# Kernel optimization log

Hardware: AMD Instinct MI355X
Metric: run time of the kernel (lower is better)

The kernel has to match this reference:

```python
import jax, jax.numpy as jnp
import numpy as np

NUM_FEATURES = 16
NUM_CLASSES = 4
HIDDEN = 128
NUM_LAYERS = 2
BN_EPS = 1e-5


def setup_inputs() -> dict:
    key = jax.random.key(0)
    ks = jax.random.split(key, 12)
    B, S, N, F, E = 8, 12, 5000, NUM_FEATURES, 40000
    H, L, C = HIDDEN, NUM_LAYERS, NUM_CLASSES
    x_seq = jax.random.normal(ks[0], (B, S, N, F), dtype=jnp.float32)
    edge_index = jax.random.randint(ks[1], (2, E), 0, N, dtype=jnp.int32)
    edge_weight = jax.random.uniform(ks[2], (E,), dtype=jnp.float32)
    def glorot(k, shape):
        fan_in, fan_out = shape[0], shape[-1]
        lim = jnp.sqrt(6.0 / (fan_in + fan_out)).astype(jnp.float32)
        return jax.random.uniform(k, shape, jnp.float32, -lim, lim)
    lin_in_W = glorot(ks[3], (F, H))
    lin_in_b = jnp.zeros((H,), jnp.float32)
    # per layer: 3 GCNConvs with weight [(H+H), H]
    convW = glorot(ks[4], (L, 3, 2 * H, H))
    convB = jnp.zeros((L, 3, H), jnp.float32)
    bn_gamma = jnp.ones((H,), jnp.float32)
    bn_beta = jnp.zeros((H,), jnp.float32)
    lin_out_W = glorot(ks[5], (H, C))
    lin_out_b = jnp.zeros((C,), jnp.float32)
    return {
        "x_seq": x_seq, "edge_index": edge_index, "edge_weight": edge_weight,
        "lin_in_W": lin_in_W, "lin_in_b": lin_in_b,
        "convW": convW, "convB": convB,
        "bn_gamma": bn_gamma, "bn_beta": bn_beta,
        "lin_out_W": lin_out_W, "lin_out_b": lin_out_b,
    }


def _batch_static_graph(edge_index, edge_weight, batch_size, num_nodes):
    E = edge_index.shape[1]
    shift = (jnp.arange(batch_size, dtype=edge_index.dtype) * num_nodes)  # [B]
    shift = jnp.repeat(shift, E)  # [B*E]
    bei = jnp.tile(edge_index, (1, batch_size)) + shift[None, :]
    bew = jnp.tile(edge_weight, batch_size)
    return bei, bew


def _gcn_norm(edge_index, edge_weight, num_nodes):
    # PyG GCNConv default: add self-loops (weight 1), sym normalization.
    loop = jnp.arange(num_nodes, dtype=edge_index.dtype)
    row = jnp.concatenate([edge_index[0], loop])
    col = jnp.concatenate([edge_index[1], loop])
    w = jnp.concatenate([edge_weight, jnp.ones((num_nodes,), edge_weight.dtype)])
    deg = jax.ops.segment_sum(w, col, num_segments=num_nodes)
    dis = jnp.where(deg > 0, jax.lax.rsqrt(jnp.where(deg > 0, deg, 1.0)), 0.0)
    norm = dis[row] * w * dis[col]
    return row, col, norm


def reference(x_seq, edge_index, edge_weight, lin_in_W, lin_in_b,
              convW, convB, bn_gamma, bn_beta, lin_out_W, lin_out_b):
    B, S, N, F = x_seq.shape
    H = lin_in_W.shape[1]
    L = convW.shape[0]
    bei, bew = _batch_static_graph(edge_index, edge_weight, B, N)
    total = B * N
    row, col, norm = _gcn_norm(bei, bew, total)
    # [S, total, F]
    xs = jnp.transpose(x_seq, (1, 0, 2, 3)).reshape(S, total, F)

    def gconv(x, W, b):
        xw = x @ W                                # [total, H]
        msg = norm[:, None] * xw[row]             # [E', H]
        return jax.ops.segment_sum(msg, col, num_segments=total) + b

    def step(h_all, x_t):
        x_t = jax.nn.relu(x_t @ lin_in_W + lin_in_b)
        new_h = []
        for l in range(L):
            h = h_all[l]
            combined = jnp.concatenate([x_t, h], axis=1)
            r = jax.nn.sigmoid(gconv(combined, convW[l, 0], convB[l, 0]))
            u = jax.nn.sigmoid(gconv(combined, convW[l, 1], convB[l, 1]))
            combined_r = jnp.concatenate([x_t, r * h], axis=1)
            c = jnp.tanh(gconv(combined_r, convW[l, 2], convB[l, 2]))
            h_new = u * h + (1.0 - u) * c
            new_h.append(h_new)
            x_t = h_new  # dropout is identity in eval mode
        return jnp.stack(new_h), None

    h0 = jnp.zeros((L, total, H), x_seq.dtype)
    h_all, _ = jax.lax.scan(step, h0, xs)
    h_final = h_all[-1]
    # BatchNorm over node dimension (training-mode batch statistics)
    mean = jnp.mean(h_final, axis=0)
    var = jnp.var(h_final, axis=0)
    h_final = (h_final - mean) * jax.lax.rsqrt(var + BN_EPS) * bn_gamma + bn_beta
    h_final = jax.nn.relu(h_final)
    out = h_final @ lin_out_W + lin_out_b            # [total, C]
    out = out.reshape(B, N, -1)
    return jax.nn.log_softmax(out, axis=-1)
```

## Files before the change

### kernel.cpp

```cpp
#include <hip/hip_runtime.h>
#include <cstdint>
#include <cstddef>

#define NN 5000
#define EE 40000
#define BATCH 8
#define SS 12
#define FF 16
#define HH 128
#define TOTAL 40000
#define CC 4


typedef __attribute__((ext_vector_type(8))) short short8;
typedef __attribute__((ext_vector_type(4))) float f32x4;

__device__ __forceinline__ unsigned short f2bf(float f) {
  union { float f; unsigned u; } v; v.f = f;
  unsigned r = v.u + 0x7fff + ((v.u >> 16) & 1);
  return (unsigned short)(r >> 16);
}
__device__ __forceinline__ float bf2f(unsigned short b) {
  union { unsigned u; float f; } v; v.u = ((unsigned)b) << 16;
  return v.f;
}
__device__ __forceinline__ float bflo(unsigned v) {
  union { unsigned u; float f; } x; x.u = v << 16; return x.f;
}
__device__ __forceinline__ float bfhi(unsigned v) {
  union { unsigned u; float f; } x; x.u = v & 0xffff0000u; return x.f;
}
__device__ __forceinline__ void qfma16(float* acc, uint4 qv, float ws) {
  unsigned wd[4] = {qv.x, qv.y, qv.z, qv.w};
#pragma unroll
  for (int d = 0; d < 4; d++) {
#pragma unroll
    for (int k = 0; k < 4; k++) {
      int q = (int)((signed char)(wd[d] >> (8 * k)));
      acc[d * 4 + k] += ws * (float)q;
    }
  }
}

__device__ __forceinline__ void gather_accum(const signed char* __restrict__ Gq,
                                             const float* __restrict__ sc,
                                             int e0, int e1,
                                             const int* __restrict__ csr_src,
                                             const float* __restrict__ csr_w,
                                             const float* __restrict__ dis,
                                             int n, int bb, int fo, float* acc) {
  float sn = dis[n]; sn *= sn;
  size_t rowSelf = (size_t)(n << 3) + bb;
#pragma unroll
  for (int k = 0; k < 16; k++) acc[k] = 0.f;
  {
    float ws = sn * sc[n];
    uint4 qv = *(const uint4*)&Gq[rowSelf * 128 + fo];
    qfma16(acc, qv, ws);
  }
  int e = e0;
  for (; e + 3 < e1; e += 4) {
    int s0 = csr_src[e], s1 = csr_src[e + 1];
    int s2 = csr_src[e + 2], s3 = csr_src[e + 3];
    float w0 = csr_w[e] * sc[s0];
    float w1 = csr_w[e + 1] * sc[s1];
    float w2 = csr_w[e + 2] * sc[s2];
    float w3 = csr_w[e + 3] * sc[s3];
    uint4 qa = *(const uint4*)&Gq[(((size_t)s0 << 3) + bb) * 128 + fo];
    uint4 qb = *(const uint4*)&Gq[(((size_t)s1 << 3) + bb) * 128 + fo];
    uint4 qc = *(const uint4*)&Gq[(((size_t)s2 << 3) + bb) * 128 + fo];
    uint4 qd = *(const uint4*)&Gq[(((size_t)s3 << 3) + bb) * 128 + fo];
    qfma16(acc, qa, w0);
    qfma16(acc, qb, w1);
    qfma16(acc, qc, w2);
    qfma16(acc, qd, w3);
  }
  for (; e < e1; e++) {
    int s0 = csr_src[e];
    float w0 = csr_w[e] * sc[s0];
    uint4 qa = *(const uint4*)&Gq[(((size_t)s0 << 3) + bb) * 128 + fo];
    qfma16(acc, qa, w0);
  }
}

__device__ __forceinline__ void gru_combine_store(const float* acc, const float* bp,
                                                  const unsigned short* __restrict__ u_in,
                                                  unsigned short* __restrict__ h_io,
                                                  size_t rowSelf, int fo,
                                                  uint4& o0, uint4& o1) {
  uint4 oo[2];
#pragma unroll
  for (int jj = 0; jj < 2; jj++) {
    uint4 uq = *(const uint4*)&u_in[rowSelf * 128 + fo + 8 * jj];
    uint4 hq = *(const uint4*)&h_io[rowSelf * 128 + fo + 8 * jj];
    float uv[8], hv[8];
    uv[0] = bflo(uq.x); uv[1] = bfhi(uq.x); uv[2] = bflo(uq.y); uv[3] = bfhi(uq.y);
    uv[4] = bflo(uq.z); uv[5] = bfhi(uq.z); uv[6] = bflo(uq.w); uv[7] = bfhi(uq.w);
    hv[0] = bflo(hq.x); hv[1] = bfhi(hq.x); hv[2] = bflo(hq.y); hv[3] = bfhi(hq.y);
    hv[4] = bflo(hq.z); hv[5] = bfhi(hq.z); hv[6] = bflo(hq.w); hv[7] = bfhi(hq.w);
    unsigned ow[4];
#pragma unroll
    for (int d = 0; d < 4; d++) {
      float v0 = acc[8 * jj + 2 * d]     + bp[8 * jj + 2 * d];
      float v1 = acc[8 * jj + 2 * d + 1] + bp[8 * jj + 2 * d + 1];
      float c0 = 1.0f - 2.0f / (__expf(2.0f * v0) + 1.0f);
      float c1 = 1.0f - 2.0f / (__expf(2.0f * v1) + 1.0f);
      float n0 = uv[2 * d] * hv[2 * d] + (1.0f - uv[2 * d]) * c0;
      float n1 = uv[2 * d + 1] * hv[2 * d + 1] + (1.0f - uv[2 * d + 1]) * c1;
      ow[d] = (unsigned)f2bf(n0) | ((unsigned)f2bf(n1) << 16);
    }
    oo[jj].x = ow[0]; oo[jj].y = ow[1]; oo[jj].z = ow[2]; oo[jj].w = ow[3];
    *(uint4*)&h_io[rowSelf * 128 + fo + 8 * jj] = oo[jj];
  }
  o0 = oo[0]; o1 = oo[1];
}


__global__ void deg_cnt_kernel(const int* __restrict__ ei, const float* __restrict__ ew,
                               float* __restrict__ deg, int* __restrict__ cnt) {
  int e = blockIdx.x * 256 + threadIdx.x;
  if (e < EE) {
    int col = ei[EE + e];
    atomicAdd(&deg[col], ew[e]);
    atomicAdd(&cnt[col], 1);
  }
}

__global__ void dis_kernel(const float* __restrict__ deg, float* __restrict__ dis) {
  int n = blockIdx.x * 256 + threadIdx.x;
  if (n < NN) dis[n] = rsqrtf(deg[n] + 1.0f);
}

__global__ void scan_kernel(const int* __restrict__ cnt, int* __restrict__ offs) {
  __shared__ int part[256];
  const int CH = (NN + 255) / 256;
  int tid = threadIdx.x;
  int base = tid * CH;
  int s = 0;
  for (int i = 0; i < CH; i++) { int idx = base + i; if (idx < NN) s += cnt[idx]; }
  part[tid] = s;
  __syncthreads();
  for (int off = 1; off < 256; off <<= 1) {
    int v = (tid >= off) ? part[tid - off] : 0;
    __syncthreads();
    part[tid] += v;
    __syncthreads();
  }
  int run = (tid == 0) ? 0 : part[tid - 1];
  for (int i = 0; i < CH; i++) {
    int idx = base + i;
    if (idx < NN) { offs[idx] = run; run += cnt[idx]; }
  }
  if (tid == 255) offs[NN] = run;
}

__global__ void fill_csr_kernel(const int* __restrict__ ei, const float* __restrict__ ew,
                                const float* __restrict__ dis, const int* __restrict__ offs,
                                int* __restrict__ cursor, int* __restrict__ csr_src,
                                float* __restrict__ csr_w) {
  int e = blockIdx.x * 256 + threadIdx.x;
  if (e < EE) {
    int row = ei[e], col = ei[EE + e];
    int pos = offs[col] + atomicAdd(&cursor[col], 1);
    csr_src[pos] = row;
    csr_w[pos] = dis[row] * ew[e] * dis[col];
  }
}


__global__ void prepack_kernel(const float* __restrict__ convW, unsigned short* __restrict__ Wp) {
  int idx = blockIdx.x * 256 + threadIdx.x;
  int lane = idx & 63;
  int ks = (idx >> 6) & 7;
  int nt = (idx >> 9) & 7;
  int g = idx >> 12;
  const float* W = convW + (size_t)g * 256 * 128;
  int n = nt * 16 + (lane & 15);
  int k0 = ks * 32 + (lane >> 4) * 8;
  unsigned short v[8];
#pragma unroll
  for (int j = 0; j < 8; j++) v[j] = f2bf(W[(size_t)(k0 + j) * 128 + n]);
  *(uint4*)(Wp + (size_t)idx * 8) = *(const uint4*)v;
}


__global__ __launch_bounds__(256) void lin_in_kernel(const float* __restrict__ x_seq,
                                                     const float* __restrict__ W,
                                                     const float* __restrict__ b,
                                                     unsigned short* __restrict__ xt, int t) {
  int idx = blockIdx.x * 256 + threadIdx.x;
  int row = idx >> 4, fh = idx & 15;
  int n = row >> 3, bb = row & 7;
  const float* xp = x_seq + (((size_t)bb * SS + t) * NN + n) * FF;
  float4 a0 = *(const float4*)&b[fh * 8];
  float4 a1 = *(const float4*)&b[fh * 8 + 4];
#pragma unroll
  for (int ff = 0; ff < FF; ff++) {
    float xv = xp[ff];
    float4 w0 = *(const float4*)&W[ff * HH + fh * 8];
    float4 w1 = *(const float4*)&W[ff * HH + fh * 8 + 4];
    a0.x += xv * w0.x; a0.y += xv * w0.y; a0.z += xv * w0.z; a0.w += xv * w0.w;
    a1.x += xv * w1.x; a1.y += xv * w1.y; a1.z += xv * w1.z; a1.w += xv * w1.w;
  }
  uint4 o;
  o.x = (unsigned)f2bf(fmaxf(a0.x, 0.f)) | ((unsigned)f2bf(fmaxf(a0.y, 0.f)) << 16);
  o.y = (unsigned)f2bf(fmaxf(a0.z, 0.f)) | ((unsigned)f2bf(fmaxf(a0.w, 0.f)) << 16);
  o.z = (unsigned)f2bf(fmaxf(a1.x, 0.f)) | ((unsigned)f2bf(fmaxf(a1.y, 0.f)) << 16);
  o.w = (unsigned)f2bf(fmaxf(a1.z, 0.f)) | ((unsigned)f2bf(fmaxf(a1.w, 0.f)) << 16);
  *(uint4*)&xt[(size_t)row * 128 + fh * 8] = o;
}


template <int MT, int NTW, int HALVES, int NTHREADS>
__device__ __forceinline__ void gemm_body(const unsigned short* As, unsigned short* Cs,
                                          float* sInv,
                                          const unsigned short* __restrict__ Wp,
                                          signed char* __restrict__ qA,
                                          signed char* __restrict__ qB,
                                          float* __restrict__ sA,
                                          float* __restrict__ sB,
                                          int rowBase, int tid) {
  constexpr int NWAVES = NTHREADS / 64;
  constexpr int NC = NTW * 16 * NWAVES;
  constexpr int R = MT * 16;
  int wv = tid >> 6, lane = tid & 63;
  int m = lane & 15, q = lane >> 4;
  f32x4 acc[MT][NTW];
#pragma unroll
  for (int i = 0; i < MT; i++)
#pragma unroll
    for (int j = 0; j < NTW; j++) acc[i][j] = (f32x4)(0.0f);
  const unsigned short* wbase = Wp + ((size_t)(wv * NTW) * 8 * 64 + lane) * 8;
#pragma unroll
  for (int ks = 0; ks < 8; ks++) {
    short8 a[MT];
#pragma unroll
    for (int mt = 0; mt < MT; mt++)
      a[mt] = *(const short8*)&As[(mt * 16 + m) * 264 + ks * 32 + q * 8];
#pragma unroll
    for (int nt = 0; nt < NTW; nt++) {
      short8 b = *(const short8*)(wbase + (size_t)(nt * 8 + ks) * 64 * 8);
#pragma unroll
      for (int mt = 0; mt < MT; mt++)
        acc[mt][nt] = __builtin_amdgcn_mfma_f32_16x16x32_bf16(a[mt], b, acc[mt][nt], 0, 0, 0);
    }
  }
  constexpr int CST = NC + 8;
#pragma unroll
  for (int mt = 0; mt < MT; mt++)
#pragma unroll
    for (int nt = 0; nt < NTW; nt++) {
      int col = (wv * NTW + nt) * 16 + m;
#pragma unroll
      for (int i = 0; i < 4; i++)
        Cs[(mt * 16 + q * 4 + i) * CST + col] = f2bf(acc[mt][nt][i]);
    }
  __syncthreads();
  constexpr int G = (R / 8) * HALVES;
  static_assert(G <= NWAVES, "one wave per quant group");
  if (wv < G) {
    int node = wv / HALVES, half = wv % HALVES;
    int c0 = half * 128 + lane * 2;
    float mx = 0.f;
#pragma unroll
    for (int r = 0; r < 8; r++) {
      const unsigned short* rp = &Cs[(node * 8 + r) * CST + c0];
      mx = fmaxf(mx, fmaxf(fabsf(bf2f(rp[0])), fabsf(bf2f(rp[1]))));
    }
#pragma unroll
    for (int off = 32; off; off >>= 1) mx = fmaxf(mx, __shfl_down(mx, off));
    if (lane == 0) {
      sInv[wv] = (mx > 0.f) ? (127.0f / mx) : 0.f;
      int gn = (rowBase >> 3) + node;
      float scv = mx * (1.0f / 127.0f);
      if (HALVES == 2) { if (half == 0) sA[gn] = scv; else sB[gn] = scv; }
      else sA[gn] = scv;
    }
  }
  __syncthreads();
  constexpr int CPQ = NC / 16;
  for (int c = tid; c < R * CPQ; c += NTHREADS) {
    int row = c / CPQ, cc = c % CPQ;
    int node = row >> 3;
    int half = (HALVES == 2) ? (cc >> 3) : 0;
    float inv = sInv[node * HALVES + half];
    const unsigned short* p = &Cs[row * CST + cc * 16];
    unsigned ow[4];
#pragma unroll
    for (int d = 0; d < 4; d++) {
      unsigned w = 0;
#pragma unroll
      for (int k = 0; k < 4; k++) {
        int qv = __float2int_rn(bf2f(p[d * 4 + k]) * inv);
        w |= ((unsigned)(qv & 255)) << (8 * k);
      }
      ow[d] = w;
    }
    signed char* dst = (half ? qB : qA) + (size_t)(rowBase + row) * 128 + (cc & 7) * 16;
    uint4 v; v.x = ow[0]; v.y = ow[1]; v.z = ow[2]; v.w = ow[3];
    *(uint4*)dst = v;
  }
}


template <int NTW, int HALVES>
__global__ __launch_bounds__(512) void gemm_mfma_q(const unsigned short* __restrict__ A1,
                                                   const unsigned short* __restrict__ A2,
                                                   const unsigned short* __restrict__ Wp,
                                                   signed char* __restrict__ qA,
                                                   signed char* __restrict__ qB,
                                                   float* __restrict__ sA,
                                                   float* __restrict__ sB) {
  __shared__ unsigned short As[32 * 264];
  __shared__ unsigned short Cs[32 * 264];
  __shared__ float sInv[8];
  int rowBase = blockIdx.x * 32;
  int tid = threadIdx.x;
  for (int c = tid; c < 1024; c += 512) {
    int row = c >> 5; int rest = c & 31; int half = rest >> 4; int sub = rest & 15;
    const unsigned short* src = (half ? A2 : A1) + ((size_t)(rowBase + row) * 128 + sub * 8);
    *(uint4*)&As[row * 264 + half * 128 + sub * 8] = *(const uint4*)src;
  }
  __syncthreads();
  gemm_body<2, NTW, HALVES, 512>(As, Cs, sInv, Wp, qA, qB, sA, sB, rowBase, tid);
}


__global__ __launch_bounds__(512, 8) void fused_cand_q(
    const signed char* __restrict__ GqR, const signed char* __restrict__ GqU,
    const float* __restrict__ sR, const float* __restrict__ sU,
    const int* __restrict__ offs, const int* __restrict__ csr_src,
    const float* __restrict__ csr_w, const float* __restrict__ dis,
    const float* __restrict__ bRU, const unsigned short* __restrict__ h,
    unsigned short* __restrict__ u_out,
    const unsigned short* __restrict__ A1, const unsigned short* __restrict__ Wp,
    signed char* __restrict__ Cq, float* __restrict__ sC) {
  __shared__ unsigned short As[32 * 264];
  __shared__ unsigned short Cs[32 * 136];
  __shared__ float sInv[8];
  int tid = threadIdx.x;
  int wv = tid >> 6, lane = tid & 63;
  int rowBase = blockIdx.x * 32, gn0 = rowBase >> 3;
  int bb = lane >> 3, fo = (lane & 7) << 4;
  int node8 = wv >> 1, half = wv & 1;
  int n = gn0 + node8;
  int e0 = offs[n], e1 = offs[n + 1];
  {
    int row = tid >> 4, sub = tid & 15;
    *(uint4*)&As[row * 264 + sub * 8] =
        *(const uint4*)&A1[(size_t)(rowBase + row) * 128 + sub * 8];
  }
  float acc[16];
  gather_accum(half ? GqU : GqR, half ? sU : sR, e0, e1, csr_src, csr_w, dis, n, bb, fo, acc);
  const float* bias = bRU + half * 128 + fo;
  size_t rowSelf = ((size_t)n << 3) + bb;
  if (half == 0) {
    int lr = node8 * 8 + bb;
#pragma unroll
    for (int jj = 0; jj < 2; jj++) {
      uint4 hq = *(const uint4*)&h[rowSelf * 128 + fo + 8 * jj];
      float hv[8];
      hv[0] = bflo(hq.x); hv[1] = bfhi(hq.x); hv[2] = bflo(hq.y); hv[3] = bfhi(hq.y);
      hv[4] = bflo(hq.z); hv[5] = bfhi(hq.z); hv[6] = bflo(hq.w); hv[7] = bfhi(hq.w);
      unsigned ow[4];
#pragma unroll
      for (int d = 0; d < 4; d++) {
        float s0 = 1.0f / (1.0f + __expf(-(acc[8 * jj + 2 * d]     + bias[8 * jj + 2 * d])));
        float s1 = 1.0f / (1.0f + __expf(-(acc[8 * jj + 2 * d + 1] + bias[8 * jj + 2 * d + 1])));
        ow[d] = (unsigned)f2bf(s0 * hv[2 * d]) | ((unsigned)f2bf(s1 * hv[2 * d + 1]) << 16);
      }
      uint4 o; o.x = ow[0]; o.y = ow[1]; o.z = ow[2]; o.w = ow[3];
      *(uint4*)&As[lr * 264 + 128 + fo + 8 * jj] = o;
    }
  } else {
#pragma unroll
    for (int jj = 0; jj < 2; jj++) {
      unsigned ow[4];
#pragma unroll
      for (int d = 0; d < 4; d++) {
        float s0 = 1.0f / (1.0f + __expf(-(acc[8 * jj + 2 * d]     + bias[8 * jj + 2 * d])));
        float s1 = 1.0f / (1.0f + __expf(-(acc[8 * jj + 2 * d + 1] + bias[8 * jj + 2 * d + 1])));
        ow[d] = (unsigned)f2bf(s0) | ((unsigned)f2bf(s1) << 16);
      }
      uint4 o; o.x = ow[0]; o.y = ow[1]; o.z = ow[2]; o.w = ow[3];
      *(uint4*)&u_out[rowSelf * 128 + fo + 8 * jj] = o;
    }
  }
  __syncthreads();
  gemm_body<2, 1, 1, 512>(As, Cs, sInv, Wp, Cq, Cq, sC, sC, rowBase, tid);
}


__global__ __launch_bounds__(512, 8) void fused_gates_q(
    const signed char* __restrict__ Cq, const float* __restrict__ sC,
    const int* __restrict__ offs, const int* __restrict__ csr_src,
    const float* __restrict__ csr_w, const float* __restrict__ dis,
    const float* __restrict__ bC, const unsigned short* __restrict__ u_in,
    unsigned short* __restrict__ h_io,
    const unsigned short* __restrict__ A2src, const unsigned short* __restrict__ Wp,
    signed char* __restrict__ GqRo, signed char* __restrict__ GqUo,
    float* __restrict__ sRo, float* __restrict__ sUo) {
  __shared__ unsigned short As[32 * 264];
  __shared__ unsigned short Cs[32 * 264];
  __shared__ float sInv[8];
  int tid = threadIdx.x;
  int wv = tid >> 6, lane = tid & 63;
  int rowBase = blockIdx.x * 32, gn0 = rowBase >> 3;
  int bb = lane >> 3, fo = (lane & 7) << 4;
  if (wv >= 4) {
    int t2 = tid - 256;
    for (int c = t2; c < 512; c += 256) {
      int row = c >> 4, sub = c & 15;
      *(uint4*)&As[row * 264 + 128 + sub * 8] =
          *(const uint4*)&A2src[(size_t)(rowBase + row) * 128 + sub * 8];
    }
  } else {
    int node8 = wv;
    int n = gn0 + node8;
    int e0 = offs[n], e1 = offs[n + 1];
    float acc[16];
    gather_accum(Cq, sC, e0, e1, csr_src, csr_w, dis, n, bb, fo, acc);
    size_t rowSelf = ((size_t)n << 3) + bb;
    uint4 o0, o1;
    gru_combine_store(acc, bC + fo, u_in, h_io, rowSelf, fo, o0, o1);
    int lr = node8 * 8 + bb;
    *(uint4*)&As[lr * 264 + fo] = o0;
    *(uint4*)&As[lr * 264 + fo + 8] = o1;
  }
  __syncthreads();
  gemm_body<2, 2, 2, 512>(As, Cs, sInv, Wp, GqRo, GqUo, sRo, sUo, rowBase, tid);
}


__global__ __launch_bounds__(512, 8) void fused_gates_lin_q(
    const signed char* __restrict__ Cq, const float* __restrict__ sC,
    const int* __restrict__ offs, const int* __restrict__ csr_src,
    const float* __restrict__ csr_w, const float* __restrict__ dis,
    const float* __restrict__ bC, const unsigned short* __restrict__ u_in,
    unsigned short* __restrict__ h_io,
    const float* __restrict__ x_seq, const float* __restrict__ Win,
    const float* __restrict__ bin, unsigned short* __restrict__ xt_out,
    const unsigned short* __restrict__ A2src, const unsigned short* __restrict__ Wp,
    signed char* __restrict__ GqRo, signed char* __restrict__ GqUo,
    float* __restrict__ sRo, float* __restrict__ sUo, int t_next) {
  __shared__ unsigned short As[32 * 264];
  __shared__ unsigned short Cs[32 * 264];
  __shared__ float sInv[8];
  int tid = threadIdx.x;
  int wv = tid >> 6, lane = tid & 63;
  int rowBase = blockIdx.x * 32, gn0 = rowBase >> 3;
  int bb = lane >> 3, fo = (lane & 7) << 4;
  if (wv < 4) {
    int node8 = wv;
    int n = gn0 + node8;
    int e0 = offs[n], e1 = offs[n + 1];
    float acc[16];
    gather_accum(Cq, sC, e0, e1, csr_src, csr_w, dis, n, bb, fo, acc);
    size_t rowSelf = ((size_t)n << 3) + bb;
    uint4 o0, o1;
    gru_combine_store(acc, bC + fo, u_in, h_io, rowSelf, fo, o0, o1);
  } else {
    int t2 = tid - 256;
    for (int c = t2; c < 512; c += 256) {
      int row = c >> 4, sub = c & 15;
      *(uint4*)&As[row * 264 + 128 + sub * 8] =
          *(const uint4*)&A2src[(size_t)(rowBase + row) * 128 + sub * 8];
    }
    for (int c = t2; c < 512; c += 256) {
      int row = c >> 4, fh = c & 15;
      int grow = rowBase + row;
      int n2 = grow >> 3, bbv = grow & 7;
      const float* xp = x_seq + (((size_t)bbv * SS + t_next) * NN + n2) * FF;
      float4 a0 = *(const float4*)&bin[fh * 8];
      float4 a1 = *(const float4*)&bin[fh * 8 + 4];
#pragma unroll
      for (int ff = 0; ff < FF; ff++) {
        float xv = xp[ff];
        float4 w0 = *(const float4*)&Win[ff * HH + fh * 8];
        float4 w1 = *(const float4*)&Win[ff * HH + fh * 8 + 4];
        a0.x += xv * w0.x; a0.y += xv * w0.y; a0.z += xv * w0.z; a0.w += xv * w0.w;
        a1.x += xv * w1.x; a1.y += xv * w1.y; a1.z += xv * w1.z; a1.w += xv * w1.w;
      }
      uint4 o;
      o.x = (unsigned)f2bf(fmaxf(a0.x, 0.f)) | ((unsigned)f2bf(fmaxf(a0.y, 0.f)) << 16);
      o.y = (unsigned)f2bf(fmaxf(a0.z, 0.f)) | ((unsigned)f2bf(fmaxf(a0.w, 0.f)) << 16);
      o.z = (unsigned)f2bf(fmaxf(a1.x, 0.f)) | ((unsigned)f2bf(fmaxf(a1.y, 0.f)) << 16);
      o.w = (unsigned)f2bf(fmaxf(a1.z, 0.f)) | ((unsigned)f2bf(fmaxf(a1.w, 0.f)) << 16);
      *(uint4*)&As[row * 264 + fh * 8] = o;
      *(uint4*)&xt_out[(size_t)grow * 128 + fh * 8] = o;
    }
  }
  __syncthreads();
  gemm_body<2, 2, 2, 512>(As, Cs, sInv, Wp, GqRo, GqUo, sRo, sUo, rowBase, tid);
}


__global__ __launch_bounds__(256) void scatter_c_update_q(
    const signed char* __restrict__ Cq, const float* __restrict__ sC,
    const int* __restrict__ offs, const int* __restrict__ csr_src,
    const float* __restrict__ csr_w, const float* __restrict__ dis,
    const float* __restrict__ bC, const unsigned short* __restrict__ u,
    unsigned short* __restrict__ h) {
  int tid = threadIdx.x;
  int wv = tid >> 6, lane = tid & 63;
  int n = blockIdx.x * 4 + wv;
  int bb = lane >> 3;
  int fo = (lane & 7) << 4;
  int e0 = offs[n], e1 = offs[n + 1];
  float acc[16];
  gather_accum(Cq, sC, e0, e1, csr_src, csr_w, dis, n, bb, fo, acc);
  size_t rowSelf = (size_t)(n << 3) + bb;
  uint4 o0, o1;
  gru_combine_store(acc, bC + fo, u, h, rowSelf, fo, o0, o1);
}


__global__ __launch_bounds__(256) void bn_stats_kernel(const unsigned short* __restrict__ h,
                                                       float* __restrict__ sums) {
  __shared__ float ls[512];
  int tid = threadIdx.x;
  float s = 0.f, sq = 0.f;
  for (size_t idx = (size_t)blockIdx.x * 256 + tid; idx < (size_t)TOTAL * HH;
       idx += (size_t)gridDim.x * 256) {
    float v = bf2f(h[idx]);
    s += v; sq += v * v;
  }
  ls[tid] = s; ls[256 + tid] = sq;
  __syncthreads();
  if (tid < 128) {
    atomicAdd(&sums[tid], ls[tid] + ls[tid + 128]);
    atomicAdd(&sums[128 + tid], ls[256 + tid] + ls[256 + tid + 128]);
  }
}


__global__ __launch_bounds__(256) void final_kernel(const unsigned short* __restrict__ h,
                                                    const float* __restrict__ sums,
                                                    const float* __restrict__ gamma,
                                                    const float* __restrict__ beta,
                                                    const float* __restrict__ Wout,
                                                    const float* __restrict__ bout,
                                                    float* __restrict__ out) {
  int wid = threadIdx.x >> 6, lane = threadIdx.x & 63;
  int row = blockIdx.x * 4 + wid;
  if (row >= TOTAL) return;
  const float inv = 1.0f / (float)TOTAL;
  float p0 = 0.f, p1 = 0.f, p2 = 0.f, p3 = 0.f;
#pragma unroll
  for (int jj = 0; jj < 2; jj++) {
    int j = lane + jj * 64;
    float mean = sums[j] * inv;
    float var = sums[128 + j] * inv - mean * mean;
    float hn = (bf2f(h[(size_t)row * HH + j]) - mean) * rsqrtf(var + 1e-5f) * gamma[j] + beta[j];
    hn = fmaxf(hn, 0.0f);
    p0 += hn * Wout[j * 4 + 0];
    p1 += hn * Wout[j * 4 + 1];
    p2 += hn * Wout[j * 4 + 2];
    p3 += hn * Wout[j * 4 + 3];
  }
  for (int off = 32; off; off >>= 1) {
    p0 += __shfl_down(p0, off);
    p1 += __shfl_down(p1, off);
    p2 += __shfl_down(p2, off);
    p3 += __shfl_down(p3, off);
  }
  if (lane == 0) {
    p0 += bout[0]; p1 += bout[1]; p2 += bout[2]; p3 += bout[3];
    float m = fmaxf(fmaxf(p0, p1), fmaxf(p2, p3));
    float e = __expf(p0 - m) + __expf(p1 - m) + __expf(p2 - m) + __expf(p3 - m);
    float lse = m + __logf(e);
    int bb = row & 7, n = row >> 3;
    float* o = out + ((size_t)bb * NN + n) * 4;
    o[0] = p0 - lse; o[1] = p1 - lse; o[2] = p2 - lse; o[3] = p3 - lse;
  }
}


extern "C" void kernel_launch(void* const* d_in, const int* in_sizes, int n_in,
                              void* d_out, int out_size, void* d_ws, size_t ws_size,
                              hipStream_t stream) {
  const float* x_seq = (const float*)d_in[0];
  const int* ei      = (const int*)d_in[1];
  const float* ew    = (const float*)d_in[2];
  const float* Win   = (const float*)d_in[3];
  const float* bin   = (const float*)d_in[4];
  const float* convW = (const float*)d_in[5];
  const float* convB = (const float*)d_in[6];
  const float* gamma = (const float*)d_in[7];
  const float* beta  = (const float*)d_in[8];
  const float* Wout  = (const float*)d_in[9];
  const float* bout  = (const float*)d_in[10];
  float* out = (float*)d_out;

  char* ws = (char*)d_ws;
  size_t off = 0;
  auto alloc = [&](size_t bytes) {
    void* p = ws + off;
    off += (bytes + 1023) & ~(size_t)1023;
    return p;
  };
  float* deg     = (float*)alloc(NN * 4);
  float* dis     = (float*)alloc(NN * 4);
  int*   cnt     = (int*)alloc(NN * 4);
  int*   offs    = (int*)alloc((NN + 1) * 4);
  int*   cursor  = (int*)alloc(NN * 4);
  int*   csr_src = (int*)alloc(EE * 4);
  float* csr_w   = (float*)alloc(EE * 4);
  float* sums    = (float*)alloc(256 * 4);
  float* sR      = (float*)alloc(NN * 4);
  float* sU      = (float*)alloc(NN * 4);
  float* sC      = (float*)alloc(NN * 4);
  unsigned short* Wp = (unsigned short*)alloc(6 * 32768 * 2);
  const size_t NH = (size_t)TOTAL * HH;
  unsigned short* h0 = (unsigned short*)alloc(NH * 2);
  unsigned short* h1 = (unsigned short*)alloc(NH * 2);
  unsigned short* xt = (unsigned short*)alloc(NH * 2);
  unsigned short* ub = (unsigned short*)alloc(NH * 2);
  signed char* GqR = (signed char*)alloc(NH);
  signed char* GqU = (signed char*)alloc(NH);
  signed char* Cq  = (signed char*)alloc(NH);

  hipMemsetAsync(deg, 0, NN * 4, stream);
  hipMemsetAsync(cnt, 0, NN * 4, stream);
  hipMemsetAsync(cursor, 0, NN * 4, stream);
  hipMemsetAsync(sums, 0, 256 * 4, stream);
  hipMemsetAsync(h0, 0, NH * 2, stream);
  hipMemsetAsync(h1, 0, NH * 2, stream);

  deg_cnt_kernel<<<(EE + 255) / 256, 256, 0, stream>>>(ei, ew, deg, cnt);
  dis_kernel<<<(NN + 255) / 256, 256, 0, stream>>>(deg, dis);
  scan_kernel<<<1, 256, 0, stream>>>(cnt, offs);
  fill_csr_kernel<<<(EE + 255) / 256, 256, 0, stream>>>(ei, ew, dis, offs, cursor, csr_src, csr_w);
  prepack_kernel<<<24576 / 256, 256, 0, stream>>>(convW, Wp);

  const unsigned short* Wg0 = Wp;
  const unsigned short* Wc0 = Wp + (size_t)2 * 32768;
  const unsigned short* Wg1 = Wp + (size_t)3 * 32768;
  const unsigned short* Wc1 = Wp + (size_t)5 * 32768;
  const float* bRU0 = convB;
  const float* bC0  = convB + 2 * HH;
  const float* bRU1 = convB + 3 * HH;
  const float* bC1  = convB + 5 * HH;

  lin_in_kernel<<<TOTAL * 16 / 256, 256, 0, stream>>>(x_seq, Win, bin, xt, 0);
  gemm_mfma_q<2, 2><<<TOTAL / 32, 512, 0, stream>>>(xt, h0, Wg0, GqR, GqU, sR, sU);

  for (int t = 0; t < SS; t++) {
    fused_cand_q<<<TOTAL / 32, 512, 0, stream>>>(GqR, GqU, sR, sU, offs, csr_src, csr_w,
                                                 dis, bRU0, h0, ub, xt, Wc0, Cq, sC);
    fused_gates_q<<<TOTAL / 32, 512, 0, stream>>>(Cq, sC, offs, csr_src, csr_w, dis,
                                                  bC0, ub, h0, h1, Wg1, GqR, GqU, sR, sU);
    fused_cand_q<<<TOTAL / 32, 512, 0, stream>>>(GqR, GqU, sR, sU, offs, csr_src, csr_w,
                                                 dis, bRU1, h1, ub, h0, Wc1, Cq, sC);
    if (t < SS - 1) {
      fused_gates_lin_q<<<TOTAL / 32, 512, 0, stream>>>(Cq, sC, offs, csr_src, csr_w, dis,
                                                        bC1, ub, h1, x_seq, Win, bin, xt,
                                                        h0, Wg0, GqR, GqU, sR, sU, t + 1);
    } else {
      scatter_c_update_q<<<NN / 4, 256, 0, stream>>>(Cq, sC, offs, csr_src, csr_w,
                                                     dis, bC1, ub, h1);
    }
  }

  bn_stats_kernel<<<256, 256, 0, stream>>>(h1, sums);
  final_kernel<<<TOTAL / 4, 256, 0, stream>>>(h1, sums, gamma, beta, Wout, bout, out);
}
```

Before: 1.539 ms.

## Defer update-gate aggregation to gates kernel and quantize directly from MFMA registers

```diff
diff --git a/kernel.cpp b/kernel.cpp
--- a/kernel.cpp
+++ b/kernel.cpp
@@ -83,19 +83,16 @@
   }
 }
 
-__device__ __forceinline__ void gru_combine_store(const float* acc, const float* bp,
-                                                  const unsigned short* __restrict__ u_in,
-                                                  unsigned short* __restrict__ h_io,
-                                                  size_t rowSelf, int fo,
-                                                  uint4& o0, uint4& o1) {
+__device__ __forceinline__ void gru_combine_f32u(const float* acc, const float* bp,
+                                                 const float* uv,
+                                                 unsigned short* __restrict__ h_io,
+                                                 size_t rowSelf, int fo,
+                                                 uint4& o0, uint4& o1) {
   uint4 oo[2];
 #pragma unroll
   for (int jj = 0; jj < 2; jj++) {
-    uint4 uq = *(const uint4*)&u_in[rowSelf * 128 + fo + 8 * jj];
     uint4 hq = *(const uint4*)&h_io[rowSelf * 128 + fo + 8 * jj];
-    float uv[8], hv[8];
-    uv[0] = bflo(uq.x); uv[1] = bfhi(uq.x); uv[2] = bflo(uq.y); uv[3] = bfhi(uq.y);
-    uv[4] = bflo(uq.z); uv[5] = bfhi(uq.z); uv[6] = bflo(uq.w); uv[7] = bfhi(uq.w);
+    float hv[8];
     hv[0] = bflo(hq.x); hv[1] = bfhi(hq.x); hv[2] = bflo(hq.y); hv[3] = bfhi(hq.y);
     hv[4] = bflo(hq.z); hv[5] = bfhi(hq.z); hv[6] = bflo(hq.w); hv[7] = bfhi(hq.w);
     unsigned ow[4];
@@ -105,8 +102,9 @@
       float v1 = acc[8 * jj + 2 * d + 1] + bp[8 * jj + 2 * d + 1];
       float c0 = 1.0f - 2.0f / (__expf(2.0f * v0) + 1.0f);
       float c1 = 1.0f - 2.0f / (__expf(2.0f * v1) + 1.0f);
-      float n0 = uv[2 * d] * hv[2 * d] + (1.0f - uv[2 * d]) * c0;
-      float n1 = uv[2 * d + 1] * hv[2 * d + 1] + (1.0f - uv[2 * d + 1]) * c1;
+      float u0 = uv[8 * jj + 2 * d], u1 = uv[8 * jj + 2 * d + 1];
+      float n0 = u0 * hv[2 * d] + (1.0f - u0) * c0;
+      float n1 = u1 * hv[2 * d + 1] + (1.0f - u1) * c1;
       ow[d] = (unsigned)f2bf(n0) | ((unsigned)f2bf(n1) << 16);
     }
     oo[jj].x = ow[0]; oo[jj].y = ow[1]; oo[jj].z = ow[2]; oo[jj].w = ow[3];
@@ -212,8 +210,7 @@
 
 
 template <int MT, int NTW, int HALVES, int NTHREADS>
-__device__ __forceinline__ void gemm_body(const unsigned short* As, unsigned short* Cs,
-                                          float* sInv,
+__device__ __forceinline__ void gemm_body(const unsigned short* As, float* gmax,
                                           const unsigned short* __restrict__ Wp,
                                           signed char* __restrict__ qA,
                                           signed char* __restrict__ qB,
@@ -221,8 +218,8 @@
                                           float* __restrict__ sB,
                                           int rowBase, int tid) {
   constexpr int NWAVES = NTHREADS / 64;
-  constexpr int NC = NTW * 16 * NWAVES;
-  constexpr int R = MT * 16;
+  constexpr int WPG = NWAVES / HALVES;
+  static_assert(MT == 2, "node mapping assumes 32-row tile");
   int wv = tid >> 6, lane = tid & 63;
   int m = lane & 15, q = lane >> 4;
   f32x4 acc[MT][NTW];
@@ -245,60 +242,55 @@
         acc[mt][nt] = __builtin_amdgcn_mfma_f32_16x16x32_bf16(a[mt], b, acc[mt][nt], 0, 0, 0);
     }
   }
-  constexpr int CST = NC + 8;
-#pragma unroll
-  for (int mt = 0; mt < MT; mt++)
+  float mxa = 0.f, mxb = 0.f;
+#pragma unroll
+  for (int nt = 0; nt < NTW; nt++)
+#pragma unroll
+    for (int i = 0; i < 4; i++) {
+      mxa = fmaxf(mxa, fabsf(acc[0][nt][i]));
+      mxb = fmaxf(mxb, fabsf(acc[1][nt][i]));
+    }
+#pragma unroll
+  for (int off = 16; off; off >>= 1) {
+    mxa = fmaxf(mxa, __shfl_down(mxa, off));
+    mxb = fmaxf(mxb, __shfl_down(mxb, off));
+  }
+  if (lane == 0)  { gmax[wv * 4 + 0] = mxa; gmax[wv * 4 + 2] = mxb; }
+  if (lane == 32) { gmax[wv * 4 + 1] = mxa; gmax[wv * 4 + 3] = mxb; }
+  __syncthreads();
+  if (tid < 4 * HALVES) {
+    int node = (HALVES == 2) ? (tid >> 1) : tid;
+    int half = (HALVES == 2) ? (tid & 1) : 0;
+    float g = 0.f;
+#pragma unroll
+    for (int w = 0; w < WPG; w++) g = fmaxf(g, gmax[(half * WPG + w) * 4 + node]);
+    float* sp = half ? sB : sA;
+    sp[(rowBase >> 3) + node] = g * (1.0f / 127.0f);
+  }
+  int half = (HALVES == 2) ? (wv / WPG) : 0;
+  int qh = q >> 1;
+  float ga = 0.f, gb = 0.f;
+#pragma unroll
+  for (int w = 0; w < WPG; w++) {
+    ga = fmaxf(ga, gmax[(half * WPG + w) * 4 + qh]);
+    gb = fmaxf(gb, gmax[(half * WPG + w) * 4 + 2 + qh]);
+  }
+  float invA = (ga > 0.f) ? (127.0f / ga) : 0.f;
+  float invB = (gb > 0.f) ? (127.0f / gb) : 0.f;
+  signed char* qbase = (half ? qB : qA);
+#pragma unroll
+  for (int mt = 0; mt < MT; mt++) {
+    float inv = mt ? invB : invA;
 #pragma unroll
     for (int nt = 0; nt < NTW; nt++) {
-      int col = (wv * NTW + nt) * 16 + m;
-#pragma unroll
-      for (int i = 0; i < 4; i++)
-        Cs[(mt * 16 + q * 4 + i) * CST + col] = f2bf(acc[mt][nt][i]);
-    }
-  __syncthreads();
-  constexpr int G = (R / 8) * HALVES;
-  static_assert(G <= NWAVES, "one wave per quant group");
-  if (wv < G) {
-    int node = wv / HALVES, half = wv % HALVES;
-    int c0 = half * 128 + lane * 2;
-    float mx = 0.f;
-#pragma unroll
-    for (int r = 0; r < 8; r++) {
-      const unsigned short* rp = &Cs[(node * 8 + r) * CST + c0];
-      mx = fmaxf(mx, fmaxf(fabsf(bf2f(rp[0])), fabsf(bf2f(rp[1]))));
-    }
-#pragma unroll
-    for (int off = 32; off; off >>= 1) mx = fmaxf(mx, __shfl_down(mx, off));
-    if (lane == 0) {
-      sInv[wv] = (mx > 0.f) ? (127.0f / mx) : 0.f;
-      int gn = (rowBase >> 3) + node;
-      float scv = mx * (1.0f / 127.0f);
-      if (HALVES == 2) { if (half == 0) sA[gn] = scv; else sB[gn] = scv; }
-      else sA[gn] = scv;
-    }
-  }
-  __syncthreads();
-  constexpr int CPQ = NC / 16;
-  for (int c = tid; c < R * CPQ; c += NTHREADS) {
-    int row = c / CPQ, cc = c % CPQ;
-    int node = row >> 3;
-    int half = (HALVES == 2) ? (cc >> 3) : 0;
-    float inv = sInv[node * HALVES + half];
-    const unsigned short* p = &Cs[row * CST + cc * 16];
-    unsigned ow[4];
-#pragma unroll
-    for (int d = 0; d < 4; d++) {
-      unsigned w = 0;
-#pragma unroll
-      for (int k = 0; k < 4; k++) {
-        int qv = __float2int_rn(bf2f(p[d * 4 + k]) * inv);
-        w |= ((unsigned)(qv & 255)) << (8 * k);
+      int colq = (wv * NTW + nt) * 16 + m - half * 128;
+      signed char* dst = qbase + (size_t)(rowBase + mt * 16 + q * 4) * 128 + colq;
+#pragma unroll
+      for (int i = 0; i < 4; i++) {
+        int qv = __float2int_rn(acc[mt][nt][i] * inv);
+        dst[(size_t)i * 128] = (signed char)qv;
       }
-      ow[d] = w;
-    }
-    signed char* dst = (half ? qB : qA) + (size_t)(rowBase + row) * 128 + (cc & 7) * 16;
-    uint4 v; v.x = ow[0]; v.y = ow[1]; v.z = ow[2]; v.w = ow[3];
-    *(uint4*)dst = v;
+    }
   }
 }
 
@@ -312,8 +304,7 @@
                                                    float* __restrict__ sA,
                                                    float* __restrict__ sB) {
   __shared__ unsigned short As[32 * 264];
-  __shared__ unsigned short Cs[32 * 264];
-  __shared__ float sInv[8];
+  __shared__ float gmax[32];
   int rowBase = blockIdx.x * 32;
   int tid = threadIdx.x;
   for (int c = tid; c < 1024; c += 512) {
@@ -322,87 +313,19 @@
     *(uint4*)&As[row * 264 + half * 128 + sub * 8] = *(const uint4*)src;
   }
   __syncthreads();
-  gemm_body<2, NTW, HALVES, 512>(As, Cs, sInv, Wp, qA, qB, sA, sB, rowBase, tid);
+  gemm_body<2, NTW, HALVES, 512>(As, gmax, Wp, qA, qB, sA, sB, rowBase, tid);
 }
 
 
 __global__ __launch_bounds__(512, 8) void fused_cand_q(
-    const signed char* __restrict__ GqR, const signed char* __restrict__ GqU,
-    const float* __restrict__ sR, const float* __restrict__ sU,
+    const signed char* __restrict__ GqR, const float* __restrict__ sR,
     const int* __restrict__ offs, const int* __restrict__ csr_src,
     const float* __restrict__ csr_w, const float* __restrict__ dis,
-    const float* __restrict__ bRU, const unsigned short* __restrict__ h,
-    unsigned short* __restrict__ u_out,
+    const float* __restrict__ bR, const unsigned short* __restrict__ h,
     const unsigned short* __restrict__ A1, const unsigned short* __restrict__ Wp,
     signed char* __restrict__ Cq, float* __restrict__ sC) {
   __shared__ unsigned short As[32 * 264];
-  __shared__ unsigned short Cs[32 * 136];
-  __shared__ float sInv[8];
-  int tid = threadIdx.x;
-  int wv = tid >> 6, lane = tid & 63;
-  int rowBase = blockIdx.x * 32, gn0 = rowBase >> 3;
-  int bb = lane >> 3, fo = (lane & 7) << 4;
-  int node8 = wv >> 1, half = wv & 1;
-  int n = gn0 + node8;
-  int e0 = offs[n], e1 = offs[n + 1];
-  {
-    int row = tid >> 4, sub = tid & 15;
-    *(uint4*)&As[row * 264 + sub * 8] =
-        *(const uint4*)&A1[(size_t)(rowBase + row) * 128 + sub * 8];
-  }
-  float acc[16];
-  gather_accum(half ? GqU : GqR, half ? sU : sR, e0, e1, csr_src, csr_w, dis, n, bb, fo, acc);
-  const float* bias = bRU + half * 128 + fo;
-  size_t rowSelf = ((size_t)n << 3) + bb;
-  if (half == 0) {
-    int lr = node8 * 8 + bb;
-#pragma unroll
-    for (int jj = 0; jj < 2; jj++) {
-      uint4 hq = *(const uint4*)&h[rowSelf * 128 + fo + 8 * jj];
-      float hv[8];
-      hv[0] = bflo(hq.x); hv[1] = bfhi(hq.x); hv[2] = bflo(hq.y); hv[3] = bfhi(hq.y);
-      hv[4] = bflo(hq.z); hv[5] = bfhi(hq.z); hv[6] = bflo(hq.w); hv[7] = bfhi(hq.w);
-      unsigned ow[4];
-#pragma unroll
-      for (int d = 0; d < 4; d++) {
-        float s0 = 1.0f / (1.0f + __expf(-(acc[8 * jj + 2 * d]     + bias[8 * jj + 2 * d])));
-        float s1 = 1.0f / (1.0f + __expf(-(acc[8 * jj + 2 * d + 1] + bias[8 * jj + 2 * d + 1])));
-        ow[d] = (unsigned)f2bf(s0 * hv[2 * d]) | ((unsigned)f2bf(s1 * hv[2 * d + 1]) << 16);
-      }
-      uint4 o; o.x = ow[0]; o.y = ow[1]; o.z = ow[2]; o.w = ow[3];
-      *(uint4*)&As[lr * 264 + 128 + fo + 8 * jj] = o;
-    }
-  } else {
-#pragma unroll
-    for (int jj = 0; jj < 2; jj++) {
-      unsigned ow[4];
-#pragma unroll
-      for (int d = 0; d < 4; d++) {
-        float s0 = 1.0f / (1.0f + __expf(-(acc[8 * jj + 2 * d]     + bias[8 * jj + 2 * d])));
-        float s1 = 1.0f / (1.0f + __expf(-(acc[8 * jj + 2 * d + 1] + bias[8 * jj + 2 * d + 1])));
-        ow[d] = (unsigned)f2bf(s0) | ((unsigned)f2bf(s1) << 16);
-      }
-      uint4 o; o.x = ow[0]; o.y = ow[1]; o.z = ow[2]; o.w = ow[3];
-      *(uint4*)&u_out[rowSelf * 128 + fo + 8 * jj] = o;
-    }
-  }
-  __syncthreads();
-  gemm_body<2, 1, 1, 512>(As, Cs, sInv, Wp, Cq, Cq, sC, sC, rowBase, tid);
-}
-
-
-__global__ __launch_bounds__(512, 8) void fused_gates_q(
-    const signed char* __restrict__ Cq, const float* __restrict__ sC,
-    const int* __restrict__ offs, const int* __restrict__ csr_src,
-    const float* __restrict__ csr_w, const float* __restrict__ dis,
-    const float* __restrict__ bC, const unsigned short* __restrict__ u_in,
-    unsigned short* __restrict__ h_io,
-    const unsigned short* __restrict__ A2src, const unsigned short* __restrict__ Wp,
-    signed char* __restrict__ GqRo, signed char* __restrict__ GqUo,
-    float* __restrict__ sRo, float* __restrict__ sUo) {
-  __shared__ unsigned short As[32 * 264];
-  __shared__ unsigned short Cs[32 * 264];
-  __shared__ float sInv[8];
+  __shared__ float gmax[32];
   int tid = threadIdx.x;
   int wv = tid >> 6, lane = tid & 63;
   int rowBase = blockIdx.x * 32, gn0 = rowBase >> 3;
@@ -411,32 +334,98 @@
     int t2 = tid - 256;
     for (int c = t2; c < 512; c += 256) {
       int row = c >> 4, sub = c & 15;
-      *(uint4*)&As[row * 264 + 128 + sub * 8] =
-          *(const uint4*)&A2src[(size_t)(rowBase + row) * 128 + sub * 8];
+      *(uint4*)&As[row * 264 + sub * 8] =
+          *(const uint4*)&A1[(size_t)(rowBase + row) * 128 + sub * 8];
     }
   } else {
     int node8 = wv;
     int n = gn0 + node8;
     int e0 = offs[n], e1 = offs[n + 1];
     float acc[16];
+    gather_accum(GqR, sR, e0, e1, csr_src, csr_w, dis, n, bb, fo, acc);
+    size_t rowSelf = ((size_t)n << 3) + bb;
+    int lr = node8 * 8 + bb;
+#pragma unroll
+    for (int jj = 0; jj < 2; jj++) {
+      uint4 hq = *(const uint4*)&h[rowSelf * 128 + fo + 8 * jj];
+      float hv[8];
+      hv[0] = bflo(hq.x); hv[1] = bfhi(hq.x); hv[2] = bflo(hq.y); hv[3] = bfhi(hq.y);
+      hv[4] = bflo(hq.z); hv[5] = bfhi(hq.z); hv[6] = bflo(hq.w); hv[7] = bfhi(hq.w);
+      unsigned ow[4];
+#pragma unroll
+      for (int d = 0; d < 4; d++) {
+        float s0 = 1.0f / (1.0f + __expf(-(acc[8 * jj + 2 * d]     + bR[fo + 8 * jj + 2 * d])));
+        float s1 = 1.0f / (1.0f + __expf(-(acc[8 * jj + 2 * d + 1] + bR[fo + 8 * jj + 2 * d + 1])));
+        ow[d] = (unsigned)f2bf(s0 * hv[2 * d]) | ((unsigned)f2bf(s1 * hv[2 * d + 1]) << 16);
+      }
+      uint4 o; o.x = ow[0]; o.y = ow[1]; o.z = ow[2]; o.w = ow[3];
+      *(uint4*)&As[lr * 264 + 128 + fo + 8 * jj] = o;
+    }
+  }
+  __syncthreads();
+  gemm_body<2, 1, 1, 512>(As, gmax, Wp, Cq, Cq, sC, sC, rowBase, tid);
+}
+
+
+__global__ __launch_bounds__(512, 8) void fused_gates_q(
+    const signed char* __restrict__ Cq, const float* __restrict__ sC,
+    const signed char* __restrict__ GqU, const float* __restrict__ sU,
+    const int* __restrict__ offs, const int* __restrict__ csr_src,
+    const float* __restrict__ csr_w, const float* __restrict__ dis,
+    const float* __restrict__ bC, const float* __restrict__ bU,
+    unsigned short* __restrict__ h_io,
+    const unsigned short* __restrict__ A2src, const unsigned short* __restrict__ Wp,
+    signed char* __restrict__ GqRo, signed char* __restrict__ GqUo,
+    float* __restrict__ sRo, float* __restrict__ sUo) {
+  __shared__ unsigned short As[32 * 264];
+  __shared__ float uls[4][64][17];
+  __shared__ float gmax[32];
+  int tid = threadIdx.x;
+  int wv = tid >> 6, lane = tid & 63;
+  int rowBase = blockIdx.x * 32, gn0 = rowBase >> 3;
+  int bb = lane >> 3, fo = (lane & 7) << 4;
+  int node8 = wv & 3;
+  int n = gn0 + node8;
+  int e0 = offs[n], e1 = offs[n + 1];
+  float acc[16];
+  if (wv < 4) {
     gather_accum(Cq, sC, e0, e1, csr_src, csr_w, dis, n, bb, fo, acc);
+  } else {
+    gather_accum(GqU, sU, e0, e1, csr_src, csr_w, dis, n, bb, fo, acc);
+#pragma unroll
+    for (int k = 0; k < 16; k++)
+      uls[node8][lane][k] = 1.0f / (1.0f + __expf(-(acc[k] + bU[fo + k])));
+  }
+  __syncthreads();
+  if (wv < 4) {
+    float uv[16];
+#pragma unroll
+    for (int k = 0; k < 16; k++) uv[k] = uls[node8][lane][k];
     size_t rowSelf = ((size_t)n << 3) + bb;
     uint4 o0, o1;
-    gru_combine_store(acc, bC + fo, u_in, h_io, rowSelf, fo, o0, o1);
+    gru_combine_f32u(acc, bC + fo, uv, h_io, rowSelf, fo, o0, o1);
     int lr = node8 * 8 + bb;
     *(uint4*)&As[lr * 264 + fo] = o0;
     *(uint4*)&As[lr * 264 + fo + 8] = o1;
-  }
-  __syncthreads();
-  gemm_body<2, 2, 2, 512>(As, Cs, sInv, Wp, GqRo, GqUo, sRo, sUo, rowBase, tid);
+  } else {
+    int t2 = tid - 256;
+    for (int c = t2; c < 512; c += 256) {
+      int row = c >> 4, sub = c & 15;
+      *(uint4*)&As[row * 264 + 128 + sub * 8] =
+          *(const uint4*)&A2src[(size_t)(rowBase + row) * 128 + sub * 8];
+    }
+  }
+  __syncthreads();
+  gemm_body<2, 2, 2, 512>(As, gmax, Wp, GqRo, GqUo, sRo, sUo, rowBase, tid);
 }
 
 
 __global__ __launch_bounds__(512, 8) void fused_gates_lin_q(
     const signed char* __restrict__ Cq, const float* __restrict__ sC,
+    const signed char* __restrict__ GqU, const float* __restrict__ sU,
     const int* __restrict__ offs, const int* __restrict__ csr_src,
     const float* __restrict__ csr_w, const float* __restrict__ dis,
-    const float* __restrict__ bC, const unsigned short* __restrict__ u_in,
+    const float* __restrict__ bC, const float* __restrict__ bU,
     unsigned short* __restrict__ h_io,
     const float* __restrict__ x_seq, const float* __restrict__ Win,
     const float* __restrict__ bin, unsigned short* __restrict__ xt_out,
@@ -444,21 +433,32 @@
     signed char* __restrict__ GqRo, signed char* __restrict__ GqUo,
     float* __restrict__ sRo, float* __restrict__ sUo, int t_next) {
   __shared__ unsigned short As[32 * 264];
-  __shared__ unsigned short Cs[32 * 264];
-  __shared__ float sInv[8];
+  __shared__ float uls[4][64][17];
+  __shared__ float gmax[32];
   int tid = threadIdx.x;
   int wv = tid >> 6, lane = tid & 63;
   int rowBase = blockIdx.x * 32, gn0 = rowBase >> 3;
   int bb = lane >> 3, fo = (lane & 7) << 4;
+  int node8 = wv & 3;
+  int n = gn0 + node8;
+  int e0 = offs[n], e1 = offs[n + 1];
+  float acc[16];
   if (wv < 4) {
-    int node8 = wv;
-    int n = gn0 + node8;
-    int e0 = offs[n], e1 = offs[n + 1];
-    float acc[16];
     gather_accum(Cq, sC, e0, e1, csr_src, csr_w, dis, n, bb, fo, acc);
+  } else {
+    gather_accum(GqU, sU, e0, e1, csr_src, csr_w, dis, n, bb, fo, acc);
+#pragma unroll
+    for (int k = 0; k < 16; k++)
+      uls[node8][lane][k] = 1.0f / (1.0f + __expf(-(acc[k] + bU[fo + k])));
+  }
+  __syncthreads();
+  if (wv < 4) {
+    float uv[16];
+#pragma unroll
+    for (int k = 0; k < 16; k++) uv[k] = uls[node8][lane][k];
     size_t rowSelf = ((size_t)n << 3) + bb;
     uint4 o0, o1;
-    gru_combine_store(acc, bC + fo, u_in, h_io, rowSelf, fo, o0, o1);
+    gru_combine_f32u(acc, bC + fo, uv, h_io, rowSelf, fo, o0, o1);
   } else {
     int t2 = tid - 256;
     for (int c = t2; c < 512; c += 256) {
@@ -491,27 +491,43 @@
     }
   }
   __syncthreads();
-  gemm_body<2, 2, 2, 512>(As, Cs, sInv, Wp, GqRo, GqUo, sRo, sUo, rowBase, tid);
-}
-
-
-__global__ __launch_bounds__(256) void scatter_c_update_q(
+  gemm_body<2, 2, 2, 512>(As, gmax, Wp, GqRo, GqUo, sRo, sUo, rowBase, tid);
+}
+
+
+__global__ __launch_bounds__(256) void scatter_c_update2(
     const signed char* __restrict__ Cq, const float* __restrict__ sC,
+    const signed char* __restrict__ GqU, const float* __restrict__ sU,
     const int* __restrict__ offs, const int* __restrict__ csr_src,
     const float* __restrict__ csr_w, const float* __restrict__ dis,
-    const float* __restrict__ bC, const unsigned short* __restrict__ u,
+    const float* __restrict__ bC, const float* __restrict__ bU,
     unsigned short* __restrict__ h) {
+  __shared__ float uls[2][64][17];
   int tid = threadIdx.x;
   int wv = tid >> 6, lane = tid & 63;
-  int n = blockIdx.x * 4 + wv;
+  int which = wv & 1;
+  int n = blockIdx.x * 2 + which;
   int bb = lane >> 3;
   int fo = (lane & 7) << 4;
   int e0 = offs[n], e1 = offs[n + 1];
   float acc[16];
-  gather_accum(Cq, sC, e0, e1, csr_src, csr_w, dis, n, bb, fo, acc);
-  size_t rowSelf = (size_t)(n << 3) + bb;
-  uint4 o0, o1;
-  gru_combine_store(acc, bC + fo, u, h, rowSelf, fo, o0, o1);
+  if (wv < 2) {
+    gather_accum(Cq, sC, e0, e1, csr_src, csr_w, dis, n, bb, fo, acc);
+  } else {
+    gather_accum(GqU, sU, e0, e1, csr_src, csr_w, dis, n, bb, fo, acc);
+#pragma unroll
+    for (int k = 0; k < 16; k++)
+      uls[which][lane][k] = 1.0f / (1.0f + __expf(-(acc[k] + bU[fo + k])));
+  }
+  __syncthreads();
+  if (wv < 2) {
+    float uv[16];
+#pragma unroll
+    for (int k = 0; k < 16; k++) uv[k] = uls[which][lane][k];
+    size_t rowSelf = (size_t)(n << 3) + bb;
+    uint4 o0, o1;
+    gru_combine_f32u(acc, bC + fo, uv, h, rowSelf, fo, o0, o1);
+  }
 }
 
 
@@ -607,18 +623,21 @@
   int*   csr_src = (int*)alloc(EE * 4);
   float* csr_w   = (float*)alloc(EE * 4);
   float* sums    = (float*)alloc(256 * 4);
-  float* sR      = (float*)alloc(NN * 4);
-  float* sU      = (float*)alloc(NN * 4);
+  float* sR0     = (float*)alloc(NN * 4);
+  float* sU0     = (float*)alloc(NN * 4);
+  float* sR1     = (float*)alloc(NN * 4);
+  float* sU1     = (float*)alloc(NN * 4);
   float* sC      = (float*)alloc(NN * 4);
   unsigned short* Wp = (unsigned short*)alloc(6 * 32768 * 2);
   const size_t NH = (size_t)TOTAL * HH;
   unsigned short* h0 = (unsigned short*)alloc(NH * 2);
   unsigned short* h1 = (unsigned short*)alloc(NH * 2);
   unsigned short* xt = (unsigned short*)alloc(NH * 2);
-  unsigned short* ub = (unsigned short*)alloc(NH * 2);
-  signed char* GqR = (signed char*)alloc(NH);
-  signed char* GqU = (signed char*)alloc(NH);
-  signed char* Cq  = (signed char*)alloc(NH);
+  signed char* GqR0 = (signed char*)alloc(NH);
+  signed char* GqU0 = (signed char*)alloc(NH);
+  signed char* GqR1 = (signed char*)alloc(NH);
+  signed char* GqU1 = (signed char*)alloc(NH);
+  signed char* Cq   = (signed char*)alloc(NH);
 
   hipMemsetAsync(deg, 0, NN * 4, stream);
   hipMemsetAsync(cnt, 0, NN * 4, stream);
@@ -637,28 +656,32 @@
   const unsigned short* Wc0 = Wp + (size_t)2 * 32768;
   const unsigned short* Wg1 = Wp + (size_t)3 * 32768;
   const unsigned short* Wc1 = Wp + (size_t)5 * 32768;
-  const float* bRU0 = convB;
-  const float* bC0  = convB + 2 * HH;
-  const float* bRU1 = convB + 3 * HH;
-  const float* bC1  = convB + 5 * HH;
+  const float* bR0 = convB;
+  const float* bU0 = convB + 128;
+  const float* bC0 = convB + 2 * HH;
+  const float* bR1 = convB + 3 * HH;
+  const float* bU1 = convB + 3 * HH + 128;
+  const float* bC1 = convB + 5 * HH;
 
   lin_in_kernel<<<TOTAL * 16 / 256, 256, 0, stream>>>(x_seq, Win, bin, xt, 0);
-  gemm_mfma_q<2, 2><<<TOTAL / 32, 512, 0, stream>>>(xt, h0, Wg0, GqR, GqU, sR, sU);
+  gemm_mfma_q<2, 2><<<TOTAL / 32, 512, 0, stream>>>(xt, h0, Wg0, GqR0, GqU0, sR0, sU0);
 
   for (int t = 0; t < SS; t++) {
-    fused_cand_q<<<TOTAL / 32, 512, 0, stream>>>(GqR, GqU, sR, sU, offs, csr_src, csr_w,
-                                                 dis, bRU0, h0, ub, xt, Wc0, Cq, sC);
-    fused_gates_q<<<TOTAL / 32, 512, 0, stream>>>(Cq, sC, offs, csr_src, csr_w, dis,
-                                                  bC0, ub, h0, h1, Wg1, GqR, GqU, sR, sU);
-    fused_cand_q<<<TOTAL / 32, 512, 0, stream>>>(GqR, GqU, sR, sU, offs, csr_src, csr_w,
-                                                 dis, bRU1, h1, ub, h0, Wc1, Cq, sC);
+    fused_cand_q<<<TOTAL / 32, 512, 0, stream>>>(GqR0, sR0, offs, csr_src, csr_w, dis,
+                                                 bR0, h0, xt, Wc0, Cq, sC);
+    fused_gates_q<<<TOTAL / 32, 512, 0, stream>>>(Cq, sC, GqU0, sU0, offs, csr_src, csr_w,
+                                                  dis, bC0, bU0, h0, h1, Wg1,
+                                                  GqR1, GqU1, sR1, sU1);
+    fused_cand_q<<<TOTAL / 32, 512, 0, stream>>>(GqR1, sR1, offs, csr_src, csr_w, dis,
+                                                 bR1, h1, h0, Wc1, Cq, sC);
     if (t < SS - 1) {
-      fused_gates_lin_q<<<TOTAL / 32, 512, 0, stream>>>(Cq, sC, offs, csr_src, csr_w, dis,
-                                                        bC1, ub, h1, x_seq, Win, bin, xt,
-                                                        h0, Wg0, GqR, GqU, sR, sU, t + 1);
+      fused_gates_lin_q<<<TOTAL / 32, 512, 0, stream>>>(Cq, sC, GqU1, sU1, offs, csr_src,
+                                                        csr_w, dis, bC1, bU1, h1,
+                                                        x_seq, Win, bin, xt, h0, Wg0,
+                                                        GqR0, GqU0, sR0, sU0, t + 1);
     } else {
-      scatter_c_update_q<<<NN / 4, 256, 0, stream>>>(Cq, sC, offs, csr_src, csr_w,
-                                                     dis, bC1, ub, h1);
+      scatter_c_update2<<<NN / 2, 256, 0, stream>>>(Cq, sC, GqU1, sU1, offs, csr_src,
+                                                    csr_w, dis, bC1, bU1, h1);
     }
   }
 
```

Result: slower. 1.634 ms (+6.1%).
